# Kernel tuning notes

Hardware: AMD Instinct MI355X
Metric: run time of the kernel (lower is better)

Reference implementation:

```python
import jax, jax.numpy as jnp
import numpy as np

B, S, D, H = 16, 2048, 1024, 1024

def setup_inputs() -> dict:
    key = jax.random.key(0)
    k1, k2, k3 = jax.random.split(key, 3)
    X = jax.random.normal(k1, (B, S, D), dtype=jnp.float32)
    W = jax.random.normal(k2, (3 * H, D), dtype=jnp.float32) * (1.0 / np.sqrt(D))
    b = jax.random.normal(k3, (3 * H,), dtype=jnp.float32) * 0.01
    return {"X": X, "W": W, "b": b}

def forget_mult(z, f):
    # z, f: [B, S, H]; h_t = z_t * f_t + (1 - f_t) * h_{t-1}, h_{-1} = 0
    z_t = jnp.moveaxis(z, 1, 0)  # [S, B, H]
    f_t = jnp.moveaxis(f, 1, 0)
    h0 = jnp.zeros(z.shape[::2], dtype=z.dtype)  # [B, H]
    def step(h, zf):
        zt, ft = zf
        h = zt * ft + (1.0 - ft) * h
        return h, h
    _, cs = jax.lax.scan(step, h0, (z_t, f_t))
    return jnp.moveaxis(cs, 0, 1)  # [B, S, H]

def reference(X, W, b):
    # window=1, output_gate=True, batch_first=True, zoneout=0, hidden=None
    Y = jnp.einsum('bsd,ed->bse', X, W) + b  # [B, S, 3H]
    z_gate, f_gate, o_gate = jnp.split(Y, 3, axis=2)
    z_gate = jnp.tanh(z_gate)
    f_gate = jax.nn.sigmoid(f_gate)
    c_gate = forget_mult(z_gate, f_gate)
    output = jax.nn.sigmoid(o_gate) * c_gate
    return output, c_gate[:, -1:]
```

## Files before the change

kernel.cpp:

```cpp
#include <hip/hip_runtime.h>
#include <hip/hip_bf16.h>
#include <hip/hip_fp16.h>


#define BB 16
#define SS 2048
#define DD 1024
#define HH 1024
#define N3 3072
#define CHUNK 64
#define NC (SS/CHUNK)

#define BM 256
#define BN 256
#define BK 64
#define NKT (DD/BK)

typedef _Float16 f16x8 __attribute__((ext_vector_type(8)));
typedef float    f32x4 __attribute__((ext_vector_type(4)));

__device__ __forceinline__ float sigm_f(float x) {
    return 1.0f / (1.0f + __expf(-x));
}
__device__ __forceinline__ float tanh_f(float x) {
    float ax = fabsf(x);
    float e  = __expf(2.0f * ax);
    float r  = 1.0f - 2.0f / (e + 1.0f);
    return copysignf(r, x);
}

__global__ __launch_bounds__(256) void cvt_f32_f16(
    const float* __restrict__ src, __half* __restrict__ dst, int n8)
{
    int i = blockIdx.x * 256 + threadIdx.x;
    if (i >= n8) return;
    const float4* s = (const float4*)src + (size_t)i * 2;
    float4 a = s[0], b = s[1];
    f16x8 v;
    v[0] = (_Float16)a.x; v[1] = (_Float16)a.y; v[2] = (_Float16)a.z; v[3] = (_Float16)a.w;
    v[4] = (_Float16)b.x; v[5] = (_Float16)b.y; v[6] = (_Float16)b.z; v[7] = (_Float16)b.w;
    *((f16x8*)dst + i) = v;
}

__global__ __launch_bounds__(512) void gemm_gates8(
    const __half* __restrict__ Xs,
    const __half* __restrict__ W16,
    const float*  __restrict__ bias,
    __half* __restrict__ G)
{
    __shared__ __half As[2][BM * BK] __attribute__((aligned(16)));
    __shared__ __half Bs[2][BN * BK] __attribute__((aligned(16)));

    const int t   = threadIdx.x;
    const int wid = t >> 6;
    const int l   = t & 63;
    const int m0  = blockIdx.x * BM;
    const int n0  = blockIdx.y * BN;
    const int wr  = wid >> 2;
    const int wc  = wid & 3;
    const int cl  = l & 15;
    const int kg  = l >> 4;
    const int cs  = cl & 7;

    f32x4 acc[8][4];
    #pragma unroll
    for (int m = 0; m < 8; ++m)
        #pragma unroll
        for (int n = 0; n < 4; ++n)
            acc[m][n] = f32x4{0.f, 0.f, 0.f, 0.f};

    const int srow = wid * 8 + (l >> 3);
    const int scol = (((l & 7) ^ ((l >> 3) & 7)) * 8);
    const __half* Xb = Xs  + (size_t)(m0 + srow) * DD + scol;
    const __half* Wb = W16 + (size_t)(n0 + srow) * DD + scol;

#define ISSUE_A(slot, j, kt) \
    __builtin_amdgcn_global_load_lds( \
        (const __attribute__((address_space(1))) void*)(Xb + (size_t)(j) * 64 * DD + (kt) * BK), \
        (__attribute__((address_space(3))) void*)(&As[slot][(j) * 4096 + wid * 512]), 16, 0, 0)
#define ISSUE_B(slot, j, kt) \
    __builtin_amdgcn_global_load_lds( \
        (const __attribute__((address_space(1))) void*)(Wb + (size_t)(j) * 64 * DD + (kt) * BK), \
        (__attribute__((address_space(3))) void*)(&Bs[slot][(j) * 4096 + wid * 512]), 16, 0, 0)

#define READ_A(ad, rh) \
    _Pragma("unroll") \
    for (int i = 0; i < 4; ++i) \
        _Pragma("unroll") \
        for (int kh = 0; kh < 2; ++kh) \
            ad[i][kh] = *(const f16x8*)(Ab + ((wr * 128 + ((rh) * 4 + i) * 16 + cl) * BK \
                                              + (((kh * 4 + kg) ^ cs) * 8)))
#define READ_B(bd, ch) \
    _Pragma("unroll") \
    for (int j = 0; j < 2; ++j) \
        _Pragma("unroll") \
        for (int kh = 0; kh < 2; ++kh) \
            bd[j][kh] = *(const f16x8*)(Bb + ((wc * 64 + ((ch) * 2 + j) * 16 + cl) * BK \
                                              + (((kh * 4 + kg) ^ cs) * 8)))

#define MFMA_Q(ad, rh, ch, bd) \
    __builtin_amdgcn_sched_barrier(0); \
    __builtin_amdgcn_s_setprio(1); \
    _Pragma("unroll") \
    for (int kh = 0; kh < 2; ++kh) \
        _Pragma("unroll") \
        for (int i = 0; i < 4; ++i) \
            _Pragma("unroll") \
            for (int j = 0; j < 2; ++j) \
                acc[(rh) * 4 + i][(ch) * 2 + j] = __builtin_amdgcn_mfma_f32_16x16x32_f16( \
                    ad[i][kh], bd[j][kh], acc[(rh) * 4 + i][(ch) * 2 + j], 0, 0, 0); \
    __builtin_amdgcn_s_setprio(0); \
    __builtin_amdgcn_sched_barrier(0)

    ISSUE_A(0, 0, 0); ISSUE_A(0, 1, 0); ISSUE_A(0, 2, 0); ISSUE_A(0, 3, 0);
    ISSUE_B(0, 0, 0); ISSUE_B(0, 1, 0); ISSUE_B(0, 2, 0); ISSUE_B(0, 3, 0);

    for (int kt = 0; kt < NKT; ++kt) {
        const int cur = kt & 1, nxt = cur ^ 1;
        const __half* Ab = As[cur];
        const __half* Bb = Bs[cur];

        if (kt + 1 < NKT) {
            ISSUE_A(nxt, 0, kt + 1); ISSUE_A(nxt, 1, kt + 1);
            ISSUE_A(nxt, 2, kt + 1); ISSUE_A(nxt, 3, kt + 1);
            ISSUE_B(nxt, 0, kt + 1); ISSUE_B(nxt, 1, kt + 1);
            ISSUE_B(nxt, 2, kt + 1); ISSUE_B(nxt, 3, kt + 1);
            asm volatile("s_waitcnt vmcnt(8)" ::: "memory");
        } else {
            asm volatile("s_waitcnt vmcnt(0)" ::: "memory");
        }
        __builtin_amdgcn_s_barrier();

        f16x8 a0[4][2], a1[4][2], b0[2][2], b1[2][2];

        READ_A(a0, 0); READ_B(b0, 0); READ_B(b1, 1);
        asm volatile("s_waitcnt lgkmcnt(4)" ::: "memory");
        MFMA_Q(a0, 0, 0, b0);
        __builtin_amdgcn_s_barrier();

        READ_A(a1, 1);
        asm volatile("s_waitcnt lgkmcnt(8)" ::: "memory");
        MFMA_Q(a0, 0, 1, b1);
        __builtin_amdgcn_s_barrier();

        asm volatile("s_waitcnt lgkmcnt(0)" ::: "memory");
        MFMA_Q(a1, 1, 1, b1);
        __builtin_amdgcn_s_barrier();

        MFMA_Q(a1, 1, 0, b0);
        __builtin_amdgcn_s_barrier();
    }
#undef MFMA_Q
#undef READ_A
#undef READ_B
#undef ISSUE_A
#undef ISSUE_B

    __half* sh = &As[0][0];
    const int bcol0 = n0 + wc * 64 + cl;
    float bv[4];
    #pragma unroll
    for (int fc = 0; fc < 4; ++fc) bv[fc] = bias[bcol0 + fc * 16];

    const int row_l = t >> 3;
    const int chunk = t & 7;

    #pragma unroll
    for (int r = 0; r < 4; ++r) {
        if (wr == (r >> 1)) {
            #pragma unroll
            for (int f4 = 0; f4 < 4; ++f4) {
                const int fr = (r & 1) * 4 + f4;
                #pragma unroll
                for (int fc = 0; fc < 4; ++fc) {
                    #pragma unroll
                    for (int i = 0; i < 4; ++i) {
                        sh[(f4 * 16 + kg * 4 + i) * 264 + wc * 64 + fc * 16 + cl] =
                            __float2half(acc[fr][fc][i] + bv[fc]);
                    }
                }
            }
        }
        __builtin_amdgcn_s_barrier();
        {
            const __half* src = sh + row_l * 264 + chunk * 32;
            __half* dst = G + (size_t)(m0 + r * 64 + row_l) * N3 + n0 + chunk * 32;
            #pragma unroll
            for (int k = 0; k < 4; ++k)
                *(f16x8*)(dst + k * 8) = *(const f16x8*)(src + k * 8);
        }
        __builtin_amdgcn_s_barrier();
    }
}

__global__ __launch_bounds__(256) void scan_pass1(
    const __half* __restrict__ G,
    float* __restrict__ Ac, float* __restrict__ Fc)
{
    const int flat = blockIdx.x * 256 + threadIdx.x;
    const int h  = flat & (HH - 1);
    const int c  = (flat >> 10) & (NC - 1);
    const int lb = flat >> 15;

    const __half* g = G + (size_t)(lb * SS + c * CHUNK) * N3 + h;
    float A = 0.f, F = 1.f;
    for (int s = 0; s < CHUNK; ++s) {
        float z = __half2float(g[0]);
        float f = __half2float(g[HH]);
        g += N3;
        float ft = sigm_f(f);
        float fp = 1.f - ft;
        A = tanh_f(z) * ft + fp * A;
        F *= fp;
    }
    Ac[flat] = A;
    Fc[flat] = F;
}

__global__ __launch_bounds__(256) void scan_pass2(
    const float* __restrict__ Ac, const float* __restrict__ Fc,
    float* __restrict__ Hin, float* __restrict__ c_last)
{
    const int flat = blockIdx.x * 256 + threadIdx.x;
    const int lb = flat >> 10;
    const int h  = flat & (HH - 1);
    float hc = 0.f;
    for (int c = 0; c < NC; ++c) {
        const size_t idx = (size_t)(lb * NC + c) * HH + h;
        Hin[idx] = hc;
        hc = Ac[idx] + Fc[idx] * hc;
    }
    c_last[flat] = hc;
}

__global__ __launch_bounds__(256) void scan_pass3(
    const __half* __restrict__ G, const float* __restrict__ Hin,
    float* __restrict__ out)
{
    const int flat = blockIdx.x * 256 + threadIdx.x;
    const int h  = flat & (HH - 1);
    const int c  = (flat >> 10) & (NC - 1);
    const int lb = flat >> 15;

    const __half* g = G + (size_t)(lb * SS + c * CHUNK) * N3 + h;
    float* o = out + (size_t)(lb * SS + c * CHUNK) * HH + h;
    float hc = Hin[flat];
    for (int s = 0; s < CHUNK; ++s) {
        float z  = __half2float(g[0]);
        float f  = __half2float(g[HH]);
        float og = __half2float(g[2 * HH]);
        g += N3;
        float ft = sigm_f(f);
        hc = tanh_f(z) * ft + (1.f - ft) * hc;
        *o = hc * sigm_f(og);
        o += HH;
    }
}

extern "C" void kernel_launch(void* const* d_in, const int* in_sizes, int n_in,
                              void* d_out, int out_size, void* d_ws, size_t ws_size,
                              hipStream_t stream) {
    const float* X    = (const float*)d_in[0];
    const float* W    = (const float*)d_in[1];
    const float* bias = (const float*)d_in[2];
    for (int i = 0; i < n_in && i < 3; ++i) {
        if      (in_sizes[i] == BB * SS * DD) X    = (const float*)d_in[i];
        else if (in_sizes[i] == N3 * DD)      W    = (const float*)d_in[i];
        else if (in_sizes[i] == N3)           bias = (const float*)d_in[i];
    }
    float* out = (float*)d_out;
    float* c_last_base = out + (size_t)BB * SS * HH;

    const size_t w16_b   = (size_t)N3 * DD * sizeof(__half);
    const size_t per_b_x = (size_t)SS * DD * sizeof(__half);
    const size_t per_b_g = (size_t)SS * N3 * sizeof(__half);
    const size_t per_b_s = (size_t)NC * HH * sizeof(float) * 3;
    int nb = 1;
    for (int cand = BB; cand >= 1; --cand) {
        if (w16_b + (size_t)cand * (per_b_x + per_b_g + per_b_s) <= ws_size) {
            nb = cand; break;
        }
    }
    if (nb > 8) nb = 8;

    __half* W16 = (__half*)d_ws;
    __half* X16 = (__half*)((char*)W16 + w16_b);
    __half* G   = (__half*)((char*)X16 + (size_t)nb * per_b_x);
    float*  Ac  = (float*)((char*)G + (size_t)nb * per_b_g);
    float*  Fc  = Ac + (size_t)nb * NC * HH;
    float*  Hin = Fc + (size_t)nb * NC * HH;

    {
        const int n8 = (N3 * DD) / 8;
        cvt_f32_f16<<<(n8 + 255) / 256, 256, 0, stream>>>(W, W16, n8);
    }

    for (int b0 = 0; b0 < BB; b0 += nb) {
        const int bs = (b0 + nb <= BB) ? nb : (BB - b0);

        const int n8x = (bs * SS * DD) / 8;
        cvt_f32_f16<<<(n8x + 255) / 256, 256, 0, stream>>>(
            X + (size_t)b0 * SS * DD, X16, n8x);

        dim3 gg(bs * (SS / BM), N3 / BN);
        gemm_gates8<<<gg, 512, 0, stream>>>(X16, W16, bias, G);

        scan_pass1<<<(bs * NC * HH) / 256, 256, 0, stream>>>(G, Ac, Fc);
        scan_pass2<<<(bs * HH) / 256, 256, 0, stream>>>(Ac, Fc, Hin,
                                                        c_last_base + (size_t)b0 * HH);
        scan_pass3<<<(bs * NC * HH) / 256, 256, 0, stream>>>(G, Hin,
                                                             out + (size_t)b0 * SS * HH);
    }
}
```

Measured before the change: 427.0 us.

## Switch GEMM to 32x32x16 MFMA, remap blocks per XCD, restagger loads

The gate GEMM now uses 32x32x16 f16 MFMA with 16-wide accumulators in place of 16x16x32, so each wave issues fewer, larger matrix ops and does fewer LDS fragment reads. The grid is flattened to 1D and block indices are remapped so consecutive blocks on the same XCD (blockIdx & 7) cover contiguous tile ranges, aiming for better L2 reuse. The B-tile prefetch is moved after the first MFMA group and most intra-iteration barriers are dropped, to overlap global loads with compute. Risks include register pressure from the larger accumulators, new LDS bank conflict patterns from the changed read layout, and a block remap that assumes the tile count divides evenly across the 8 XCDs.

```diff
diff --git a/kernel.cpp b/kernel.cpp
--- a/kernel.cpp
+++ b/kernel.cpp
@@ -16,8 +16,8 @@
 #define BK 64
 #define NKT (DD/BK)
 
-typedef _Float16 f16x8 __attribute__((ext_vector_type(8)));
-typedef float    f32x4 __attribute__((ext_vector_type(4)));
+typedef _Float16 f16x8  __attribute__((ext_vector_type(8)));
+typedef float    f32x16 __attribute__((ext_vector_type(16)));
 
 __device__ __forceinline__ float sigm_f(float x) {
     return 1.0f / (1.0f + __expf(-x));
@@ -46,28 +46,34 @@
     const __half* __restrict__ Xs,
     const __half* __restrict__ W16,
     const float*  __restrict__ bias,
-    __half* __restrict__ G)
+    __half* __restrict__ G,
+    int mtiles)
 {
     __shared__ __half As[2][BM * BK] __attribute__((aligned(16)));
     __shared__ __half Bs[2][BN * BK] __attribute__((aligned(16)));
+
+    const int q   = (mtiles * 3) >> 1;
+    const int sb  = (blockIdx.x & 7) * q + (blockIdx.x >> 3);
+    const int m0  = (sb % mtiles) * BM;
+    const int n0  = (sb / mtiles) * BN;
 
     const int t   = threadIdx.x;
     const int wid = t >> 6;
     const int l   = t & 63;
-    const int m0  = blockIdx.x * BM;
-    const int n0  = blockIdx.y * BN;
     const int wr  = wid >> 2;
     const int wc  = wid & 3;
-    const int cl  = l & 15;
-    const int kg  = l >> 4;
-    const int cs  = cl & 7;
-
-    f32x4 acc[8][4];
+    const int l31 = l & 31;
+    const int lh  = l >> 5;
+    const int cs  = l & 7;
+
+    f32x16 acc[4][2];
     #pragma unroll
-    for (int m = 0; m < 8; ++m)
+    for (int m = 0; m < 4; ++m)
         #pragma unroll
-        for (int n = 0; n < 4; ++n)
-            acc[m][n] = f32x4{0.f, 0.f, 0.f, 0.f};
+        for (int n = 0; n < 2; ++n)
+            #pragma unroll
+            for (int e = 0; e < 16; ++e)
+                acc[m][n][e] = 0.f;
 
     const int srow = wid * 8 + (l >> 3);
     const int scol = (((l & 7) ^ ((l >> 3) & 7)) * 8);
@@ -83,32 +89,28 @@
         (const __attribute__((address_space(1))) void*)(Wb + (size_t)(j) * 64 * DD + (kt) * BK), \
         (__attribute__((address_space(3))) void*)(&Bs[slot][(j) * 4096 + wid * 512]), 16, 0, 0)
 
-#define READ_A(ad, rh) \
+#define READ_A(ad, mh) \
     _Pragma("unroll") \
-    for (int i = 0; i < 4; ++i) \
+    for (int mf2 = 0; mf2 < 2; ++mf2) \
         _Pragma("unroll") \
-        for (int kh = 0; kh < 2; ++kh) \
-            ad[i][kh] = *(const f16x8*)(Ab + ((wr * 128 + ((rh) * 4 + i) * 16 + cl) * BK \
-                                              + (((kh * 4 + kg) ^ cs) * 8)))
-#define READ_B(bd, ch) \
+        for (int ks = 0; ks < 4; ++ks) \
+            ad[mf2][ks] = *(const f16x8*)(Ab + ((wr * 128 + ((mh) * 2 + mf2) * 32 + l31) * BK \
+                                                + (((ks * 2 + lh) ^ cs) * 8)))
+#define READ_B(bd, nf) \
     _Pragma("unroll") \
-    for (int j = 0; j < 2; ++j) \
-        _Pragma("unroll") \
-        for (int kh = 0; kh < 2; ++kh) \
-            bd[j][kh] = *(const f16x8*)(Bb + ((wc * 64 + ((ch) * 2 + j) * 16 + cl) * BK \
-                                              + (((kh * 4 + kg) ^ cs) * 8)))
-
-#define MFMA_Q(ad, rh, ch, bd) \
+    for (int ks = 0; ks < 4; ++ks) \
+        bd[ks] = *(const f16x8*)(Bb + ((wc * 64 + (nf) * 32 + l31) * BK \
+                                       + (((ks * 2 + lh) ^ cs) * 8)))
+
+#define MFMA_Q(ad, mh, nf, bd) \
     __builtin_amdgcn_sched_barrier(0); \
     __builtin_amdgcn_s_setprio(1); \
     _Pragma("unroll") \
-    for (int kh = 0; kh < 2; ++kh) \
+    for (int ks = 0; ks < 4; ++ks) \
         _Pragma("unroll") \
-        for (int i = 0; i < 4; ++i) \
-            _Pragma("unroll") \
-            for (int j = 0; j < 2; ++j) \
-                acc[(rh) * 4 + i][(ch) * 2 + j] = __builtin_amdgcn_mfma_f32_16x16x32_f16( \
-                    ad[i][kh], bd[j][kh], acc[(rh) * 4 + i][(ch) * 2 + j], 0, 0, 0); \
+        for (int mf2 = 0; mf2 < 2; ++mf2) \
+            acc[(mh) * 2 + mf2][nf] = __builtin_amdgcn_mfma_f32_32x32x16_f16( \
+                ad[mf2][ks], bd[ks], acc[(mh) * 2 + mf2][nf], 0, 0, 0); \
     __builtin_amdgcn_s_setprio(0); \
     __builtin_amdgcn_sched_barrier(0)
 
@@ -123,31 +125,32 @@
         if (kt + 1 < NKT) {
             ISSUE_A(nxt, 0, kt + 1); ISSUE_A(nxt, 1, kt + 1);
             ISSUE_A(nxt, 2, kt + 1); ISSUE_A(nxt, 3, kt + 1);
+            asm volatile("s_waitcnt vmcnt(4)" ::: "memory");
+        } else {
+            asm volatile("s_waitcnt vmcnt(0)" ::: "memory");
+        }
+        __builtin_amdgcn_s_barrier();
+
+        f16x8 a0[2][4], a1[2][4], b0[4], b1[4];
+
+        READ_A(a0, 0); READ_B(b0, 0);
+        asm volatile("s_waitcnt lgkmcnt(0)" ::: "memory");
+        MFMA_Q(a0, 0, 0, b0);
+
+        READ_B(b1, 1);
+        if (kt + 1 < NKT) {
             ISSUE_B(nxt, 0, kt + 1); ISSUE_B(nxt, 1, kt + 1);
             ISSUE_B(nxt, 2, kt + 1); ISSUE_B(nxt, 3, kt + 1);
-            asm volatile("s_waitcnt vmcnt(8)" ::: "memory");
-        } else {
-            asm volatile("s_waitcnt vmcnt(0)" ::: "memory");
-        }
-        __builtin_amdgcn_s_barrier();
-
-        f16x8 a0[4][2], a1[4][2], b0[2][2], b1[2][2];
-
-        READ_A(a0, 0); READ_B(b0, 0); READ_B(b1, 1);
-        asm volatile("s_waitcnt lgkmcnt(4)" ::: "memory");
-        MFMA_Q(a0, 0, 0, b0);
-        __builtin_amdgcn_s_barrier();
+        }
+        asm volatile("s_waitcnt lgkmcnt(0)" ::: "memory");
+        MFMA_Q(a0, 0, 1, b1);
 
         READ_A(a1, 1);
-        asm volatile("s_waitcnt lgkmcnt(8)" ::: "memory");
-        MFMA_Q(a0, 0, 1, b1);
-        __builtin_amdgcn_s_barrier();
-
         asm volatile("s_waitcnt lgkmcnt(0)" ::: "memory");
         MFMA_Q(a1, 1, 1, b1);
-        __builtin_amdgcn_s_barrier();
 
         MFMA_Q(a1, 1, 0, b0);
+
         __builtin_amdgcn_s_barrier();
     }
 #undef MFMA_Q
@@ -157,10 +160,9 @@
 #undef ISSUE_B
 
     __half* sh = &As[0][0];
-    const int bcol0 = n0 + wc * 64 + cl;
-    float bv[4];
+    float bvn[2];
     #pragma unroll
-    for (int fc = 0; fc < 4; ++fc) bv[fc] = bias[bcol0 + fc * 16];
+    for (int nf = 0; nf < 2; ++nf) bvn[nf] = bias[n0 + wc * 64 + nf * 32 + l31];
 
     const int row_l = t >> 3;
     const int chunk = t & 7;
@@ -169,14 +171,15 @@
     for (int r = 0; r < 4; ++r) {
         if (wr == (r >> 1)) {
             #pragma unroll
-            for (int f4 = 0; f4 < 4; ++f4) {
-                const int fr = (r & 1) * 4 + f4;
+            for (int mf2 = 0; mf2 < 2; ++mf2) {
+                const int mf = (r & 1) * 2 + mf2;
                 #pragma unroll
-                for (int fc = 0; fc < 4; ++fc) {
+                for (int nf = 0; nf < 2; ++nf) {
                     #pragma unroll
-                    for (int i = 0; i < 4; ++i) {
-                        sh[(f4 * 16 + kg * 4 + i) * 264 + wc * 64 + fc * 16 + cl] =
-                            __float2half(acc[fr][fc][i] + bv[fc]);
+                    for (int reg = 0; reg < 16; ++reg) {
+                        const int rl = mf2 * 32 + (reg & 3) + 8 * (reg >> 2) + 4 * lh;
+                        sh[rl * 264 + wc * 64 + nf * 32 + l31] =
+                            __float2half(acc[mf][nf][reg] + bvn[nf]);
                     }
                 }
             }
@@ -302,8 +305,8 @@
         cvt_f32_f16<<<(n8x + 255) / 256, 256, 0, stream>>>(
             X + (size_t)b0 * SS * DD, X16, n8x);
 
-        dim3 gg(bs * (SS / BM), N3 / BN);
-        gemm_gates8<<<gg, 512, 0, stream>>>(X16, W16, bias, G);
+        const int mtiles = bs * (SS / BM);
+        gemm_gates8<<<mtiles * 12, 512, 0, stream>>>(X16, W16, bias, G, mtiles);
 
         scan_pass1<<<(bs * NC * HH) / 256, 256, 0, stream>>>(G, Ac, Fc);
         scan_pass2<<<(bs * HH) / 256, 256, 0, stream>>>(Ac, Fc, Hin,
```

After: 456.4 us. +6.9%, slower.
